# Kernel tuning notes

Hardware: AMD Instinct MI355X
Metric: run time of the kernel (lower is better)

The kernel has to match this reference:

```python
import jax, jax.numpy as jnp
import numpy as np

N_EXP = 8
TOP_K = 2
CAPACITY_FACTOR = 1.25


def setup_inputs() -> dict:
    key = jax.random.key(0)
    ks = jax.random.split(key, 5)
    B, T, D = 4, 1024, 1024
    H = 4 * D
    E = N_EXP
    x = jax.random.normal(ks[0], (B, T, D), jnp.float32)
    gate_w = jax.random.normal(ks[1], (D, E), jnp.float32) * 0.02
    c_fc = jax.random.normal(ks[2], (E, D, H), jnp.float32) * 0.02
    fc_bias = jnp.zeros((E, 1, H), jnp.float32)
    c_proj = jax.random.normal(ks[3], (E, H, D), jnp.float32) * 0.02
    proj_bias = jnp.zeros((E, 1, D), jnp.float32)
    return dict(x=x, gate_w=gate_w, c_fc=c_fc, fc_bias=fc_bias,
                c_proj=c_proj, proj_bias=proj_bias)


def reference(x, gate_w, c_fc, fc_bias, c_proj, proj_bias):
    B, T, D = x.shape
    n = B * T
    E, k = N_EXP, TOP_K
    cap = int(CAPACITY_FACTOR * n * k / E)  # expert capacity

    xt = x.reshape(n, D)

    # ---- Router ----
    logits = xt @ gate_w                                   # [n, E]
    top_logits, top_idx = jax.lax.top_k(logits, k)         # [n, k]
    # softmax over only the top-k experts (others set to -inf)
    masked = jnp.full_like(logits, -jnp.inf)
    masked = masked.at[jnp.arange(n)[:, None], top_idx].set(top_logits)
    router_probs = jax.nn.softmax(masked, axis=-1)         # [n, E]

    exp_mask = jax.nn.one_hot(top_idx, E, dtype=jnp.int32)  # [n, k, E]
    exp_mask = jnp.transpose(exp_mask, (1, 0, 2))           # [k, n, E]

    # rank of each token within its expert's batch (k=0 choices first)
    exp_rank = jnp.cumsum(exp_mask.reshape(k * n, E), axis=0) - 1
    exp_rank = exp_rank.reshape(k, n, E)

    # drop tokens exceeding capacity
    exp_mask = exp_mask * (exp_rank < cap).astype(jnp.int32)
    used_capacity = jnp.sum(exp_mask, axis=(0, 1))          # [E]

    exp_rank = jnp.sum(exp_mask * exp_rank, axis=-1)        # [k, n] slot index

    exp_weights = exp_mask.astype(x.dtype) * router_probs[None]  # [k, n, E]
    rank_oh = jax.nn.one_hot(exp_rank, cap, dtype=x.dtype)        # [k, n, cap]

    # combine weights [n, E, cap]
    cb_weight = jnp.einsum('kne,knc->nec', exp_weights, rank_oh)
    sec_mask = (cb_weight != 0).astype(x.dtype)             # dispatch mask

    # ---- Dispatch: one-hot matmul -> per-expert batches ----
    exp_batches = jnp.einsum('nec,nd->ecd', sec_mask, xt)   # [E, cap, D]

    # ---- Expert MLP (batched GEMMs, exact GELU, dropout=0/eval) ----
    h = jnp.einsum('ecd,edh->ech', exp_batches, c_fc) + fc_bias
    h = jax.nn.gelu(h, approximate=False)
    exp_out = jnp.einsum('ech,ehd->ecd', h, c_proj) + proj_bias  # [E, cap, D]

    # ---- Combine ----
    out = jnp.einsum('nec,ecd->nd', cb_weight, exp_out)     # [n, D]
    return out.reshape(B, T, D)
```

## Files before the change

### kernel.cpp

```cpp
#include <hip/hip_runtime.h>
#include <hip/hip_bf16.h>

typedef unsigned short u16;
typedef unsigned int u32;

#define N_TOK 4096
#define DIM   1024
#define HID   4096
#define N_EXP 8
#define CAP   1280

typedef short short8 __attribute__((ext_vector_type(8)));
typedef float f32x4 __attribute__((ext_vector_type(4)));

__device__ __forceinline__ u16 bf16rne(float f) {
    u32 u = __float_as_uint(f);
    u32 r = u + 0x7FFFu + ((u >> 16) & 1u);
    return (u16)(r >> 16);
}
__device__ __forceinline__ float bf2f(u16 h) {
    return __uint_as_float(((u32)h) << 16);
}

#define GLDS(gp, lp) __builtin_amdgcn_global_load_lds( \
    (const __attribute__((address_space(1))) void*)(gp), \
    (__attribute__((address_space(3))) void*)(lp), 16, 0, 0)

__global__ void router_kernel(const float* __restrict__ x,
                              const float* __restrict__ gw,
                              int* __restrict__ r_eidx,
                              float* __restrict__ r_w) {
    const int wave = threadIdx.x >> 6, lane = threadIdx.x & 63;
    const int t = blockIdx.x * 4 + wave;
    const float* xr = x + (size_t)t * DIM;
    float acc[8];
#pragma unroll
    for (int e = 0; e < 8; e++) acc[e] = 0.f;
#pragma unroll 4
    for (int i = 0; i < DIM / 64; i++) {
        int d = i * 64 + lane;
        float xv = xr[d];
        const float4* g = (const float4*)(gw + (size_t)d * 8);
        float4 g0 = g[0], g1 = g[1];
        acc[0] += xv * g0.x; acc[1] += xv * g0.y;
        acc[2] += xv * g0.z; acc[3] += xv * g0.w;
        acc[4] += xv * g1.x; acc[5] += xv * g1.y;
        acc[6] += xv * g1.z; acc[7] += xv * g1.w;
    }
#pragma unroll
    for (int e = 0; e < 8; e++) {
#pragma unroll
        for (int off = 32; off > 0; off >>= 1)
            acc[e] += __shfl_xor(acc[e], off, 64);
    }
    if (lane == 0) {
        int e0 = 0; float l0 = acc[0];
#pragma unroll
        for (int e = 1; e < 8; e++) if (acc[e] > l0) { l0 = acc[e]; e0 = e; }
        int e1 = -1; float l1 = -1e30f;
#pragma unroll
        for (int e = 0; e < 8; e++) if (e != e0 && acc[e] > l1) { l1 = acc[e]; e1 = e; }
        float z = __expf(l1 - l0);
        float inv = 1.f / (1.f + z);
        r_eidx[t] = e0; r_eidx[N_TOK + t] = e1;
        r_w[t] = inv;   r_w[N_TOK + t] = z * inv;
    }
}

__global__ void assign_kernel(const int* __restrict__ r_eidx,
                              int* __restrict__ assign_slot,
                              int* __restrict__ token_for_slot,
                              int* __restrict__ used) {
    const int tid = threadIdx.x;
    __shared__ int wtot[8][16];
    __shared__ int wbase[8][16];
    for (int i = tid; i < N_EXP * CAP; i += 1024) token_for_slot[i] = -1;

    int le[8], lr[8], cnt[8];
#pragma unroll
    for (int e = 0; e < 8; e++) cnt[e] = 0;
#pragma unroll
    for (int j = 0; j < 8; j++) {
        int e = r_eidx[tid * 8 + j];
        le[j] = e;
        int r = 0;
#pragma unroll
        for (int e2 = 0; e2 < 8; e2++)
            if (e == e2) { r = cnt[e2]; cnt[e2] = r + 1; }
        lr[j] = r;
    }
    const int lane = tid & 63, wv = tid >> 6;
    int excl[8];
#pragma unroll
    for (int e = 0; e < 8; e++) {
        int v = cnt[e], inc = v;
#pragma unroll
        for (int off = 1; off < 64; off <<= 1) {
            int u = __shfl_up(inc, off, 64);
            if (lane >= off) inc += u;
        }
        excl[e] = inc - v;
        if (lane == 63) wtot[e][wv] = inc;
    }
    __syncthreads();
    if (tid < 8) {
        int s = 0;
        for (int w = 0; w < 16; w++) { wbase[tid][w] = s; s += wtot[tid][w]; }
        used[tid] = s < CAP ? s : CAP;
    }
    __syncthreads();
#pragma unroll
    for (int j = 0; j < 8; j++) {
        int i = tid * 8 + j;
        int e = le[j];
        int b = 0;
#pragma unroll
        for (int e2 = 0; e2 < 8; e2++)
            if (e == e2) b = wbase[e2][wv] + excl[e2];
        int rank = b + lr[j];
        int tok = i & (N_TOK - 1);
        if (rank < CAP) {
            assign_slot[i] = rank;
            token_for_slot[e * CAP + rank] = tok;
        } else {
            assign_slot[i] = -1;
        }
    }
}

__global__ void gather_kernel(const float* __restrict__ x,
                              const int* __restrict__ token_for_slot,
                              u16* __restrict__ exp_batches) {
    const int s = blockIdx.x;
    const int tok = token_for_slot[s];
    const int d = threadIdx.x * 4;
    ushort4 o;
    if (tok >= 0) {
        float4 v = *(const float4*)(x + (size_t)tok * DIM + d);
        o = make_ushort4(bf16rne(v.x), bf16rne(v.y), bf16rne(v.z), bf16rne(v.w));
    } else {
        o = make_ushort4(0, 0, 0, 0);
    }
    *(ushort4*)(exp_batches + (size_t)s * DIM + d) = o;
}

__global__ __launch_bounds__(256) void transpose_cvt(
    const float* __restrict__ in, u16* __restrict__ out, int R, int C) {
    __shared__ float t[64][65];
    const int ez = blockIdx.z;
    in  += (size_t)ez * R * C;
    out += (size_t)ez * R * C;
    const int row0 = blockIdx.y * 64, col0 = blockIdx.x * 64;
    const int tid = threadIdx.x;
    {
        const int r = tid >> 2, cq = (tid & 3) * 16;
        const float* p = in + (size_t)(row0 + r) * C + col0 + cq;
        float4 v0 = ((const float4*)p)[0];
        float4 v1 = ((const float4*)p)[1];
        float4 v2 = ((const float4*)p)[2];
        float4 v3 = ((const float4*)p)[3];
        float tmp[16] = {v0.x, v0.y, v0.z, v0.w, v1.x, v1.y, v1.z, v1.w,
                         v2.x, v2.y, v2.z, v2.w, v3.x, v3.y, v3.z, v3.w};
#pragma unroll
        for (int j = 0; j < 16; j++) t[r][cq + j] = tmp[j];
    }
    __syncthreads();
    {
        const int oc = tid >> 2, h4 = (tid & 3) * 16;
        u16 o[16];
#pragma unroll
        for (int i = 0; i < 16; i++) o[i] = bf16rne(t[h4 + i][oc]);
        u16* q = out + (size_t)(col0 + oc) * R + row0 + h4;
        *(uint4*)q = *(const uint4*)&o[0];
        *(uint4*)(q + 8) = *(const uint4*)&o[8];
    }
}

template <bool DO_GELU>
__global__ __launch_bounds__(512, 2) void moe_gemm8(
    const u16* __restrict__ A, const u16* __restrict__ Bt,
    const float* __restrict__ bias, u16* __restrict__ C,
    const int* __restrict__ used, int N, int K) {
    __shared__ __align__(16) u16 lds[4][2][8192];

    const int NT = K >> 5;
    const int bid = blockIdx.x;
    const int e = bid & 7;
    const int local = bid >> 3;
    const int row0 = (local % (CAP / 256)) * 256;
    const int col0 = (local / (CAP / 256)) * 256;
    if (row0 >= used[e]) return;

    A    += (size_t)e * CAP * K;
    Bt   += (size_t)e * N * K;
    bias += (size_t)e * N;
    C    += (size_t)e * CAP * N;

    const int tid = threadIdx.x;
    const int lane = tid & 63, wave = tid >> 6;
    const int wr128 = (wave >> 2) * 128;
    const int wc64  = (wave & 3) * 64;

    const int opB = wave >> 2;
    const int rg  = wave & 3;
    const u16* gp = opB ? (Bt + (size_t)(col0 + rg * 64 + lane) * K)
                        : (A  + (size_t)(row0 + rg * 64 + lane) * K);

    f32x4 acc[8][4];
#pragma unroll
    for (int i = 0; i < 8; i++)
#pragma unroll
        for (int j = 0; j < 4; j++) acc[i][j] = (f32x4){0.f, 0.f, 0.f, 0.f};

#pragma unroll
    for (int u = 0; u < 3; ++u)
#pragma unroll
        for (int k8 = 0; k8 < 4; ++k8)
            GLDS(gp + u * 32 + k8 * 8, &lds[u][opB][k8 * 2048 + rg * 512]);
    asm volatile("s_waitcnt vmcnt(8)" ::: "memory");
    asm volatile("s_barrier" ::: "memory");

    const int rrd  = lane & 15;
    const int qoff = (lane >> 4) * 2048;

    for (int t = 0; t < NT; ++t) {
        const u16* As_s = &lds[t & 3][0][0];
        const u16* Bs_s = &lds[t & 3][1][0];
        const int  t3 = t + 3;
        const bool st = t3 < NT;
        u16* dst = &lds[t3 & 3][opB][rg * 512];
        const u16* src = gp + (size_t)t3 * 32;

        short8 af[4], bfr[4];
#pragma unroll
        for (int j = 0; j < 4; ++j)
            bfr[j] = *(const short8*)(Bs_s + qoff + (wc64 + j * 16 + rrd) * 8);
#pragma unroll
        for (int i = 0; i < 4; ++i)
            af[i] = *(const short8*)(As_s + qoff + (wr128 + i * 16 + rrd) * 8);
        if (st) { GLDS(src, dst); GLDS(src + 8, dst + 2048); }
        asm volatile("s_barrier" ::: "memory");
        __builtin_amdgcn_s_setprio(1);
#pragma unroll
        for (int i = 0; i < 4; ++i)
#pragma unroll
            for (int j = 0; j < 4; ++j)
                acc[i][j] = __builtin_amdgcn_mfma_f32_16x16x32_bf16(
                    af[i], bfr[j], acc[i][j], 0, 0, 0);
        __builtin_amdgcn_s_setprio(0);
        asm volatile("s_barrier" ::: "memory");
#pragma unroll
        for (int i = 0; i < 4; ++i)
            af[i] = *(const short8*)(As_s + qoff + (wr128 + 64 + i * 16 + rrd) * 8);
        if (st) { GLDS(src + 16, dst + 4096); GLDS(src + 24, dst + 6144); }
        asm volatile("s_barrier" ::: "memory");
        __builtin_amdgcn_s_setprio(1);
#pragma unroll
        for (int i = 0; i < 4; ++i)
#pragma unroll
            for (int j = 0; j < 4; ++j)
                acc[4 + i][j] = __builtin_amdgcn_mfma_f32_16x16x32_bf16(
                    af[i], bfr[j], acc[4 + i][j], 0, 0, 0);
        __builtin_amdgcn_s_setprio(0);
        if (t < NT - 3)       asm volatile("s_waitcnt vmcnt(8)" ::: "memory");
        else if (t == NT - 3) asm volatile("s_waitcnt vmcnt(4)" ::: "memory");
        else if (t == NT - 2) asm volatile("s_waitcnt vmcnt(0)" ::: "memory");
        asm volatile("s_barrier" ::: "memory");
    }

    const int cr = (lane >> 4) * 4;
    const int cc = lane & 15;
#pragma unroll
    for (int j = 0; j < 4; ++j) {
        const int col = col0 + wc64 + j * 16 + cc;
        const float bv = bias[col];
#pragma unroll
        for (int i = 0; i < 8; ++i) {
#pragma unroll
            for (int r = 0; r < 4; ++r) {
                int row = row0 + wr128 + i * 16 + cr + r;
                float v = acc[i][j][r] + bv;
                if (DO_GELU) {
                    float u = 0.7978845608f * v * (1.f + 0.044715f * v * v);
                    v = v / (1.f + __expf(-2.f * u));
                }
                C[(size_t)row * N + col] = bf16rne(v);
            }
        }
    }
}

__global__ void combine_kernel(const int* __restrict__ r_eidx,
                               const float* __restrict__ r_w,
                               const int* __restrict__ assign_slot,
                               const u16* __restrict__ exp_out,
                               float* __restrict__ out) {
    const int t = blockIdx.x;
    const int d = threadIdx.x * 4;
    const int e0 = r_eidx[t], e1 = r_eidx[N_TOK + t];
    const float w0 = r_w[t], w1 = r_w[N_TOK + t];
    const int s0 = assign_slot[t], s1 = assign_slot[N_TOK + t];
    float v0 = 0.f, v1 = 0.f, v2 = 0.f, v3 = 0.f;
    if (s0 >= 0) {
        const u16* p = exp_out + ((size_t)e0 * CAP + s0) * DIM + d;
        ushort4 q = *(const ushort4*)p;
        v0 += w0 * bf2f(q.x); v1 += w0 * bf2f(q.y);
        v2 += w0 * bf2f(q.z); v3 += w0 * bf2f(q.w);
    }
    if (s1 >= 0) {
        const u16* p = exp_out + ((size_t)e1 * CAP + s1) * DIM + d;
        ushort4 q = *(const ushort4*)p;
        v0 += w1 * bf2f(q.x); v1 += w1 * bf2f(q.y);
        v2 += w1 * bf2f(q.z); v3 += w1 * bf2f(q.w);
    }
    float4 o; o.x = v0; o.y = v1; o.z = v2; o.w = v3;
    *(float4*)(out + (size_t)t * DIM + d) = o;
}

extern "C" void kernel_launch(void* const* d_in, const int* in_sizes, int n_in,
                              void* d_out, int out_size, void* d_ws, size_t ws_size,
                              hipStream_t stream) {
    const float* x         = (const float*)d_in[0];
    const float* gate_w    = (const float*)d_in[1];
    const float* c_fc      = (const float*)d_in[2];
    const float* fc_bias   = (const float*)d_in[3];
    const float* c_proj    = (const float*)d_in[4];
    const float* proj_bias = (const float*)d_in[5];
    float* out = (float*)d_out;
    char* ws = (char*)d_ws;

    int*   r_eidx         = (int*)(ws + 0);
    float* r_w            = (float*)(ws + 32768);
    int*   assign_slot    = (int*)(ws + 65536);
    int*   token_for_slot = (int*)(ws + 98304);
    int*   used           = (int*)(ws + 139264);
    u16*   exp_batches    = (u16*)(ws + 163840);
    u16*   exp_out        = exp_batches;
    u16*   h              = (u16*)(ws + 21135360);
    u16*   Bt             = (u16*)(ws + 105021440);

    router_kernel<<<N_TOK / 4, 256, 0, stream>>>(x, gate_w, r_eidx, r_w);
    assign_kernel<<<1, 1024, 0, stream>>>(r_eidx, assign_slot, token_for_slot, used);
    gather_kernel<<<N_EXP * CAP, 256, 0, stream>>>(x, token_for_slot, exp_batches);

    transpose_cvt<<<dim3(HID / 64, DIM / 64, N_EXP), 256, 0, stream>>>(
        c_fc, Bt, DIM, HID);
    moe_gemm8<true><<<(HID / 256) * (CAP / 256) * N_EXP, 512, 0, stream>>>(
        exp_batches, Bt, fc_bias, h, used, HID, DIM);

    transpose_cvt<<<dim3(DIM / 64, HID / 64, N_EXP), 256, 0, stream>>>(
        c_proj, Bt, HID, DIM);
    moe_gemm8<false><<<(DIM / 256) * (CAP / 256) * N_EXP, 512, 0, stream>>>(
        h, Bt, proj_bias, exp_out, used, DIM, HID);

    combine_kernel<<<N_TOK, 256, 0, stream>>>(r_eidx, r_w, assign_slot, exp_out, out);
}
```

Before: 657.1 us.

## Rewrite expert GEMM with K=64 double-buffered swizzled LDS and templated row tile

```diff
diff --git a/kernel.cpp b/kernel.cpp
--- a/kernel.cpp
+++ b/kernel.cpp
@@ -25,6 +25,12 @@
 #define GLDS(gp, lp) __builtin_amdgcn_global_load_lds( \
     (const __attribute__((address_space(1))) void*)(gp), \
     (__attribute__((address_space(3))) void*)(lp), 16, 0, 0)
+
+#define SBAR  asm volatile("s_barrier" ::: "memory")
+#define LGKM0 asm volatile("s_waitcnt lgkmcnt(0)" ::: "memory")
+#define VMW8  asm volatile("s_waitcnt vmcnt(8)" ::: "memory")
+#define VMW5  asm volatile("s_waitcnt vmcnt(5)" ::: "memory")
+#define VMW0  asm volatile("s_waitcnt vmcnt(0)" ::: "memory")
 
 __global__ void router_kernel(const float* __restrict__ x,
                               const float* __restrict__ gw,
@@ -176,19 +182,23 @@
     }
 }
 
-template <bool DO_GELU>
-__global__ __launch_bounds__(512, 2) void moe_gemm8(
+template <int BM, bool DO_GELU>
+__global__ __launch_bounds__(512, 2) void moe_gemm256(
     const u16* __restrict__ A, const u16* __restrict__ Bt,
     const float* __restrict__ bias, u16* __restrict__ C,
     const int* __restrict__ used, int N, int K) {
-    __shared__ __align__(16) u16 lds[4][2][8192];
-
-    const int NT = K >> 5;
+    constexpr int MI   = BM / 32;
+    constexpr int ALW  = BM / 32;
+    constexpr int BUFE = (BM + 256) * 64;
+    constexpr int NROW = CAP / BM;
+    __shared__ __align__(16) u16 lds[2 * BUFE];
+
+    const int NT = K >> 6;
     const int bid = blockIdx.x;
     const int e = bid & 7;
     const int local = bid >> 3;
-    const int row0 = (local % (CAP / 256)) * 256;
-    const int col0 = (local / (CAP / 256)) * 256;
+    const int row0 = (local % NROW) * BM;
+    const int col0 = (local / NROW) * 256;
     if (row0 >= used[e]) return;
 
     A    += (size_t)e * CAP * K;
@@ -198,93 +208,109 @@
 
     const int tid = threadIdx.x;
     const int lane = tid & 63, wave = tid >> 6;
-    const int wr128 = (wave >> 2) * 128;
-    const int wc64  = (wave & 3) * 64;
-
-    const int opB = wave >> 2;
-    const int rg  = wave & 3;
-    const u16* gp = opB ? (Bt + (size_t)(col0 + rg * 64 + lane) * K)
-                        : (A  + (size_t)(row0 + rg * 64 + lane) * K);
-
-    f32x4 acc[8][4];
-#pragma unroll
-    for (int i = 0; i < 8; i++)
+    const int mh   = wave >> 2;
+    const int wv4  = wave & 3;
+    const int wr   = mh * (BM / 2);
+    const int wc64 = wv4 * 64;
+
+    const int srow = lane >> 3;
+    const int swz  = ((lane & 7) ^ srow) * 8;
+    const int LW   = mh ? 8 : ALW;
+    const int ro0  = wv4 * LW * 8;
+    const u16* gsrc = (mh ? Bt + (size_t)(col0 + ro0 + srow) * K
+                          : A  + (size_t)(row0 + ro0 + srow) * K) + swz;
+    u16* dbase = lds + (mh ? BM * 64 : 0) + ro0 * 64;
+
+    auto stage = [&](int buf, int kt) {
+        u16* db = dbase + (size_t)buf * BUFE;
+        const u16* sb = gsrc + kt;
+        if (mh) {
+#pragma unroll
+            for (int i = 0; i < 8; ++i)
+                GLDS(sb + (size_t)(i * 8) * K, db + i * 512);
+        } else {
+#pragma unroll
+            for (int i = 0; i < ALW; ++i)
+                GLDS(sb + (size_t)(i * 8) * K, db + i * 512);
+        }
+    };
+    auto waitL = [&]() {
+        if constexpr (ALW == 8) { VMW8; }
+        else { if (mh) { VMW8; } else { VMW5; } }
+    };
+
+    f32x4 acc[MI][4];
+#pragma unroll
+    for (int i = 0; i < MI; i++)
 #pragma unroll
         for (int j = 0; j < 4; j++) acc[i][j] = (f32x4){0.f, 0.f, 0.f, 0.f};
 
-#pragma unroll
-    for (int u = 0; u < 3; ++u)
-#pragma unroll
-        for (int k8 = 0; k8 < 4; ++k8)
-            GLDS(gp + u * 32 + k8 * 8, &lds[u][opB][k8 * 2048 + rg * 512]);
-    asm volatile("s_waitcnt vmcnt(8)" ::: "memory");
-    asm volatile("s_barrier" ::: "memory");
-
-    const int rrd  = lane & 15;
-    const int qoff = (lane >> 4) * 2048;
+    stage(0, 0);
+    stage(1, 64);
+    waitL();
+    SBAR;
+
+    const int rrd = lane & 15, qrd = lane >> 4;
+    const int k0 = ((qrd ^ (rrd & 7)) << 3);
+    const int k1 = (((4 + qrd) ^ (rrd & 7)) << 3);
+    const int aoff = (wr + rrd) * 64;
+    const int boff = (wc64 + rrd) * 64;
 
     for (int t = 0; t < NT; ++t) {
-        const u16* As_s = &lds[t & 3][0][0];
-        const u16* Bs_s = &lds[t & 3][1][0];
-        const int  t3 = t + 3;
-        const bool st = t3 < NT;
-        u16* dst = &lds[t3 & 3][opB][rg * 512];
-        const u16* src = gp + (size_t)t3 * 32;
-
-        short8 af[4], bfr[4];
-#pragma unroll
-        for (int j = 0; j < 4; ++j)
-            bfr[j] = *(const short8*)(Bs_s + qoff + (wc64 + j * 16 + rrd) * 8);
-#pragma unroll
-        for (int i = 0; i < 4; ++i)
-            af[i] = *(const short8*)(As_s + qoff + (wr128 + i * 16 + rrd) * 8);
-        if (st) { GLDS(src, dst); GLDS(src + 8, dst + 2048); }
-        asm volatile("s_barrier" ::: "memory");
-        __builtin_amdgcn_s_setprio(1);
-#pragma unroll
-        for (int i = 0; i < 4; ++i)
+        const u16* As = lds + (size_t)(t & 1) * BUFE;
+        const u16* Bs = As + BM * 64;
+
+        short8 bf0[4], bf1[4];
+#pragma unroll
+        for (int j = 0; j < 4; ++j) {
+            bf0[j] = *(const short8*)(Bs + boff + j * 1024 + k0);
+            bf1[j] = *(const short8*)(Bs + boff + j * 1024 + k1);
+        }
+#pragma unroll
+        for (int i = 0; i < MI; ++i) {
+            short8 a0 = *(const short8*)(As + aoff + i * 1024 + k0);
+            short8 a1 = *(const short8*)(As + aoff + i * 1024 + k1);
+            __builtin_amdgcn_s_setprio(1);
 #pragma unroll
             for (int j = 0; j < 4; ++j)
                 acc[i][j] = __builtin_amdgcn_mfma_f32_16x16x32_bf16(
-                    af[i], bfr[j], acc[i][j], 0, 0, 0);
-        __builtin_amdgcn_s_setprio(0);
-        asm volatile("s_barrier" ::: "memory");
-#pragma unroll
-        for (int i = 0; i < 4; ++i)
-            af[i] = *(const short8*)(As_s + qoff + (wr128 + 64 + i * 16 + rrd) * 8);
-        if (st) { GLDS(src + 16, dst + 4096); GLDS(src + 24, dst + 6144); }
-        asm volatile("s_barrier" ::: "memory");
-        __builtin_amdgcn_s_setprio(1);
-#pragma unroll
-        for (int i = 0; i < 4; ++i)
+                    a0, bf0[j], acc[i][j], 0, 0, 0);
 #pragma unroll
             for (int j = 0; j < 4; ++j)
-                acc[4 + i][j] = __builtin_amdgcn_mfma_f32_16x16x32_bf16(
-                    af[i], bfr[j], acc[4 + i][j], 0, 0, 0);
-        __builtin_amdgcn_s_setprio(0);
-        if (t < NT - 3)       asm volatile("s_waitcnt vmcnt(8)" ::: "memory");
-        else if (t == NT - 3) asm volatile("s_waitcnt vmcnt(4)" ::: "memory");
-        else if (t == NT - 2) asm volatile("s_waitcnt vmcnt(0)" ::: "memory");
-        asm volatile("s_barrier" ::: "memory");
-    }
-
-    const int cr = (lane >> 4) * 4;
-    const int cc = lane & 15;
-#pragma unroll
-    for (int j = 0; j < 4; ++j) {
-        const int col = col0 + wc64 + j * 16 + cc;
-        const float bv = bias[col];
-#pragma unroll
-        for (int i = 0; i < 8; ++i) {
-#pragma unroll
-            for (int r = 0; r < 4; ++r) {
-                int row = row0 + wr128 + i * 16 + cr + r;
-                float v = acc[i][j][r] + bv;
+                acc[i][j] = __builtin_amdgcn_mfma_f32_16x16x32_bf16(
+                    a1, bf1[j], acc[i][j], 0, 0, 0);
+            __builtin_amdgcn_s_setprio(0);
+        }
+
+        if (t < NT - 1) {
+            LGKM0;
+            __builtin_amdgcn_sched_barrier(0);
+            SBAR;
+            if (t + 2 < NT) { stage(t & 1, (t + 2) * 64); waitL(); }
+            else            { VMW0; }
+            SBAR;
+        }
+    }
+
+    const int cr = qrd * 4;
+    const int cc = rrd;
+    float bv[4];
+#pragma unroll
+    for (int j = 0; j < 4; ++j) bv[j] = bias[col0 + wc64 + j * 16 + cc];
+#pragma unroll
+    for (int i = 0; i < MI; ++i) {
+#pragma unroll
+        for (int r = 0; r < 4; ++r) {
+            const int row = row0 + wr + i * 16 + cr + r;
+            u16* cp = C + (size_t)row * N + col0 + wc64 + cc;
+#pragma unroll
+            for (int j = 0; j < 4; ++j) {
+                float v = acc[i][j][r] + bv[j];
                 if (DO_GELU) {
                     float u = 0.7978845608f * v * (1.f + 0.044715f * v * v);
                     v = v / (1.f + __expf(-2.f * u));
                 }
-                C[(size_t)row * N + col] = bf16rne(v);
+                cp[j * 16] = bf16rne(v);
             }
         }
     }
@@ -345,12 +371,12 @@
 
     transpose_cvt<<<dim3(HID / 64, DIM / 64, N_EXP), 256, 0, stream>>>(
         c_fc, Bt, DIM, HID);
-    moe_gemm8<true><<<(HID / 256) * (CAP / 256) * N_EXP, 512, 0, stream>>>(
+    moe_gemm256<256, true><<<(CAP / 256) * (HID / 256) * N_EXP, 512, 0, stream>>>(
         exp_batches, Bt, fc_bias, h, used, HID, DIM);
 
     transpose_cvt<<<dim3(DIM / 64, HID / 64, N_EXP), 256, 0, stream>>>(
         c_proj, Bt, HID, DIM);
-    moe_gemm8<false><<<(DIM / 256) * (CAP / 256) * N_EXP, 512, 0, stream>>>(
+    moe_gemm256<160, false><<<(CAP / 160) * (DIM / 256) * N_EXP, 512, 0, stream>>>(
         h, Bt, proj_bias, exp_out, used, DIM, HID);
 
     combine_kernel<<<N_TOK, 256, 0, stream>>>(r_eidx, r_w, assign_slot, exp_out, out);
```

Measured after the change: 559.7 us. 14.8% less time.
